# Optimization experiments

Measured on AMD Instinct MI355X. Metric: run time of the kernel, lower is better.

The kernel has to match this reference:

```python
import jax, jax.numpy as jnp
import numpy as np

B, CIN, COUT, N = 8, 64, 64, 4096
MODES, L, M = 64, 100, 20


def _cc_nodes_weights(m):
    # Clenshaw-Curtis nodes cos(k*pi/n) and weights on [-1, 1]
    n = m - 1
    k = np.arange(m)
    nodes = np.cos(np.pi * k / n)
    v = np.ones(m)
    for j in range(1, n // 2 + 1):
        b = 1.0 if 2 * j == n else 2.0
        v -= b / (4.0 * j * j - 1.0) * np.cos(2.0 * j * k * np.pi / n)
    w = 2.0 * v / n
    w[0] *= 0.5
    w[-1] *= 0.5
    return nodes, w


def setup_inputs() -> dict:
    key = jax.random.key(0)
    k1, k2, k3 = jax.random.split(key, 3)
    scale = 1.0 / (CIN * COUT)
    x = jax.random.normal(k1, (B, CIN, N), dtype=jnp.float32)
    w_real = scale * jax.random.uniform(k2, (CIN, COUT, MODES), dtype=jnp.float32)
    w_imag = scale * jax.random.uniform(k3, (CIN, COUT, MODES), dtype=jnp.float32)
    return {"x": x, "w_real": w_real, "w_imag": w_imag}


def _forward(x, w_real, w_imag):
    b, c, n = x.shape
    t = jnp.linspace(0.0, 1.0, n)
    f = np.fft.fftfreq(n, d=1.0 / n).astype(np.float32)  # integer freqs, fft order
    nodes, cw = _cc_nodes_weights(M)

    # ---- CFT: X(f) = sum_{segments l, cheb nodes k} w_lk * x(t_lk) * exp(-2i*pi*f*t_lk)
    h = 0.5 / L                               # segment half-width on [0,1]
    cents = (np.arange(L) + 0.5) / L
    t_nodes = (cents[:, None] + h * nodes[None, :]).ravel().astype(np.float32)  # (L*M,)
    wts = np.broadcast_to(h * cw, (L, M)).ravel().astype(np.float32)            # (L*M,)
    tq = jnp.asarray(t_nodes)
    # interpolate each (b, c) signal onto the Chebyshev quadrature nodes
    xs = jax.vmap(lambda s: jnp.interp(tq, t, s))(x.reshape(b * c, n))  # (BC, LM)
    phase = -2.0 * jnp.pi * jnp.asarray(f)[:, None] * tq[None, :]       # (N, LM)
    E = jnp.exp(1j * phase).astype(jnp.complex64) * jnp.asarray(wts)[None, :]
    x_cft = (xs.astype(jnp.complex64) @ E.T).reshape(b, c, n)           # (B, Cin, N)

    # ---- spectral channel mixing on lowest MODES fft-order frequencies
    w = (w_real + 1j * w_imag).astype(jnp.complex64)
    out_low = jnp.einsum('bix,iox->box', x_cft[:, :, :MODES], w)
    out_ft = jnp.concatenate(
        [out_low, jnp.zeros((b, COUT, n - MODES), dtype=jnp.complex64)], axis=-1)

    # ---- ICFT: x(t) = int X(f) exp(+2i*pi*f*t) df via the same segment quadrature
    order = np.argsort(f)
    f_sorted = f[order]
    cs = out_ft[:, :, jnp.asarray(order)].reshape(b * COUT, n)
    fa, fb = float(f_sorted[0]), float(f_sorted[-1])
    hf = (fb - fa) / (2.0 * L)
    fc = fa + (np.arange(L) + 0.5) * (fb - fa) / L
    f_nodes = (fc[:, None] + hf * nodes[None, :]).ravel().astype(np.float32)
    wfs = np.broadcast_to(hf * cw, (L, M)).ravel().astype(np.float32)
    fq = jnp.asarray(f_nodes)
    fs = jnp.asarray(f_sorted)
    ci = jax.vmap(lambda cv: jnp.interp(fq, fs, cv.real)
                  + 1j * jnp.interp(fq, fs, cv.imag))(cs)               # (BC, LM)
    phase2 = 2.0 * jnp.pi * fq[:, None] * t[None, :]                     # (LM, N)
    E2 = jnp.exp(1j * phase2).astype(jnp.complex64) * jnp.asarray(wfs)[:, None]
    return (ci.astype(jnp.complex64) @ E2).real.reshape(b, COUT, n)


def reference(x, w_real, w_imag):
    return _forward(x, w_real, w_imag)
```

## Files before the change

kernel.cpp:

```cpp
#include <hip/hip_runtime.h>


#define NN 4096
#define C1_19 0.9863613034027223
#define NS3 33
#define NSP 40
#define MAGIC 0x7fc0deadu

#define OFF_XRE 0
#define OFF_XIM 32768
#define OFF_Z   65536

__device__ __forceinline__ float sin_rev(float r) { return __builtin_amdgcn_sinf(r); }
__device__ __forceinline__ float cos_rev(float r) { return __builtin_amdgcn_cosf(r); }

__device__ __forceinline__ void build_tables(double* nd, double* cwd, int t) {
    if (t == 0) {
        nd[0] = 1.0; nd[1] = C1_19;
        for (int k = 2; k < 20; ++k) nd[k] = 2.0 * C1_19 * nd[k - 1] - nd[k - 2];
    }
    __syncthreads();
    if (t < 20) {
        double v = 1.0;
        for (int j = 1; j <= 9; ++j) {
            int q = (2 * j * t) % 38; if (q > 19) q = 38 - q;
            v -= 2.0 / (4.0 * j * j - 1.0) * nd[q];
        }
        double w = 2.0 * v / 19.0;
        if (t == 0 || t == 19) w *= 0.5;
        cwd[t] = w;
    }
}

struct PA { float xs[NN]; float xq[2000]; float Fri[20][64][2]; float red[4][64][2]; };
struct PB { float wsl[2][64][64]; float part[4][2][64]; float yt[2][64]; };
union SU { PA a; PB b; };

__global__ __launch_bounds__(256, 4) void k_cftmix(const float* __restrict__ x,
                                                   const float* __restrict__ wr,
                                                   const float* __restrict__ wi,
                                                   float* __restrict__ ws,
                                                   float* __restrict__ out) {
    __shared__ SU su;
    __shared__ double nd[20], cwd[20];
    __shared__ float sw0[NS3], sw1[NS3];
    __shared__ int   si0[NS3], si1[NS3];
    const int t = threadIdx.x;
    const int vb = blockIdx.x;

    if (vb < 512) {
        const int bc = vb;
        build_tables(nd, cwd, t);
#pragma unroll
        for (int it = 0; it < 4; ++it) {
            int c4 = it * 256 + t;
            *(float4*)&su.a.xs[c4 * 4] = *(const float4*)&x[(size_t)bc * NN + c4 * 4];
        }
        __syncthreads();
        for (int idx = t; idx < 1280; idx += 256) {
            int k = idx >> 6, m = idx & 63;
            double r = -0.005 * nd[k] * (double)m;
            r -= floor(r);
            float fr = (float)r;
            float w = (float)(0.005 * cwd[k]);
            su.a.Fri[k][m][0] = w * cos_rev(fr);
            su.a.Fri[k][m][1] = w * sin_rev(fr);
        }
#pragma unroll
        for (int it = 0; it < 8; ++it) {
            int node = it * 256 + t;
            if (node < 2000) {
                int l = node / 20, k = node - l * 20;
                double tq = 0.005 * ((double)(2 * l + 1) + nd[k]);
                double sf = tq * 4095.0;
                int i = (int)sf; if (i > 4094) i = 4094;
                double a = sf - (double)i;
                if (a < 0.0) a = 0.0; if (a > 1.0) a = 1.0;
                float af = (float)a;
                su.a.xq[node] = (1.f - af) * su.a.xs[i] + af * su.a.xs[i + 1];
            }
        }
        __syncthreads();
        const int m = t & 63, grp = t >> 6;
        float Fre[20], Fim[20];
#pragma unroll
        for (int k = 0; k < 20; ++k) {
            Fre[k] = su.a.Fri[k][m][0];
            Fim[k] = su.a.Fri[k][m][1];
        }
        float ar = 0.f, ai = 0.f;
        for (int l = grp * 25; l < grp * 25 + 25; ++l) {
            const float4* q4 = (const float4*)&su.a.xq[l * 20];
            float ur = 0.f, ui = 0.f;
#pragma unroll
            for (int c = 0; c < 5; ++c) {
                float4 q = q4[c];
                ur += q.x * Fre[c * 4]     + q.y * Fre[c * 4 + 1]
                    + q.z * Fre[c * 4 + 2] + q.w * Fre[c * 4 + 3];
                ui += q.x * Fim[c * 4]     + q.y * Fim[c * 4 + 1]
                    + q.z * Fim[c * 4 + 2] + q.w * Fim[c * 4 + 3];
            }
            int u = (m * (2 * l + 1)) % 200;
            float fr = (float)u * 0.005f;
            float tr = cos_rev(fr), ti = -sin_rev(fr);
            ar += tr * ur - ti * ui;
            ai += tr * ui + ti * ur;
        }
        su.a.red[grp][m][0] = ar;
        su.a.red[grp][m][1] = ai;
        __syncthreads();
        if (t < 64) {
            float sr = (su.a.red[0][t][0] + su.a.red[1][t][0]) +
                       (su.a.red[2][t][0] + su.a.red[3][t][0]);
            float si = (su.a.red[0][t][1] + su.a.red[1][t][1]) +
                       (su.a.red[2][t][1] + su.a.red[3][t][1]);
            __hip_atomic_store(&ws[OFF_XRE + (size_t)bc * 64 + t], sr,
                               __ATOMIC_RELAXED, __HIP_MEMORY_SCOPE_SYSTEM);
            __hip_atomic_store(&ws[OFF_XIM + (size_t)bc * 64 + t], si,
                               __ATOMIC_RELAXED, __HIP_MEMORY_SCOPE_SYSTEM);
        }
        __syncthreads();
        if (t == 0)
            __hip_atomic_store((unsigned*)out + (size_t)bc * 16, MAGIC,
                               __ATOMIC_RELAXED, __HIP_MEMORY_SCOPE_SYSTEM);
    } else {
        const int id = vb - 512;
        const int b = id >> 6, o = id & 63;
        build_tables(nd, cwd, t);
        __syncthreads();
        if (t < NS3) {
            int l = (t < 2) ? 49 : (t < 22 ? 50 : 51);
            int k = (t < 2) ? t : (t < 22 ? t - 2 : t - 13);
            double fq = -2048.0 + ((double)l + 0.5) * 40.95 + 20.475 * nd[k];
            int m0 = (int)floor(fq);
            float fr = (float)(fq - (double)m0);
            sw0[t] = (m0 >= 0 && m0 <= 63) ? (1.f - fr) : 0.f;
            sw1[t] = (m0 + 1 >= 0 && m0 + 1 <= 63) ? fr : 0.f;
            si0[t] = min(max(m0, 0), 63);
            si1[t] = min(max(m0 + 1, 0), 63);
        }
        for (int idx = t; idx < 2048; idx += 256) {
            int arr = idx >> 10, rem = idx & 1023;
            int i = rem >> 4, c4 = rem & 15;
            const float* src = arr ? wi : wr;
            *(float4*)&su.b.wsl[arr][i][c4 * 4] =
                *(const float4*)&src[(((size_t)i * 64 + o) << 6) + c4 * 4];
        }
        if (t < 64) {
            const unsigned* fp = (const unsigned*)out + (size_t)(b * 64 + t) * 16;
            while (__hip_atomic_load(fp, __ATOMIC_RELAXED,
                                     __HIP_MEMORY_SCOPE_SYSTEM) != MAGIC)
                __builtin_amdgcn_s_sleep(2);
        }
        __syncthreads();
        const int m = t & 63, grp = t >> 6;
        float yr = 0.f, yi = 0.f;
#pragma unroll 4
        for (int i = grp * 16; i < grp * 16 + 16; ++i) {
            const size_t off = (size_t)(b * 64 + i) * 64 + m;
            float xr = ws[OFF_XRE + off];
            float xi = ws[OFF_XIM + off];
            float a = su.b.wsl[0][i][m];
            float c = su.b.wsl[1][i][m];
            yr += xr * a - xi * c;
            yi += xr * c + xi * a;
        }
        su.b.part[grp][0][m] = yr;
        su.b.part[grp][1][m] = yi;
        __syncthreads();
        if (t < 128) {
            int pr = t >> 6, mm = t & 63;
            su.b.yt[pr][mm] = ((su.b.part[0][pr][mm] + su.b.part[1][pr][mm]) +
                               (su.b.part[2][pr][mm] + su.b.part[3][pr][mm]));
        }
        __syncthreads();
        if (t < 2 * NS3) {
            int p = t >= NS3, s = t - p * NS3;
            float z = sw0[s] * su.b.yt[p][si0[s]] + sw1[s] * su.b.yt[p][si1[s]];
            ws[OFF_Z + (size_t)p * 512 * NSP + ((size_t)b * 64 + o) * NSP + s] = z;
        } else if (t < 2 * NS3 + 14) {
            int q = t - 2 * NS3;
            int p = q / 7, s = NS3 + q % 7;
            ws[OFF_Z + (size_t)p * 512 * NSP + ((size_t)b * 64 + o) * NSP + s] = 0.f;
        }
    }
}

__global__ __launch_bounds__(256) void k_icft(const float* __restrict__ ws,
                                              float* __restrict__ out) {
    __shared__ double nd[20], cwd[20];
    __shared__ double sfq[NS3];
    __shared__ float  swf[NS3];
    __shared__ __align__(16) float zt[2][64][41];
    __shared__ __align__(16) float e2[2][NSP][36];
    const int t = threadIdx.x;
    const int jt2 = blockIdx.x, pc = blockIdx.y;
    build_tables(nd, cwd, t);
    __syncthreads();
    if (t < NS3) {
        int l = (t < 2) ? 49 : (t < 22 ? 50 : 51);
        int k = (t < 2) ? t : (t < 22 ? t - 2 : t - 13);
        sfq[t] = -2048.0 + ((double)l + 0.5) * 40.95 + 20.475 * nd[k];
        swf[t] = (float)(20.475 * cwd[k]);
    }
    for (int idx = t; idx < 2 * 64 * NSP; idx += 256) {
        int part = idx / (64 * NSP), rem = idx % (64 * NSP);
        int row = rem / NSP, s = rem % NSP;
        zt[part][row][s] =
            ws[OFF_Z + (size_t)part * 512 * NSP + ((size_t)pc * 64 + row) * NSP + s];
    }
    __syncthreads();
    const double inv4095 = 1.0 / 4095.0;
    for (int idx = t; idx < NSP * 32; idx += 256) {
        int s = idx >> 5, jl = idx & 31;
        float cr = 0.f, ci = 0.f;
        if (s < NS3) {
            double ph = sfq[s] * ((double)(jt2 * 32 + jl) * inv4095);
            ph -= floor(ph);
            float fr = (float)ph;
            cr = swf[s] * cos_rev(fr);
            ci = swf[s] * sin_rev(fr);
        }
        e2[0][s][jl] = cr;
        e2[1][s][jl] = ci;
    }
    __syncthreads();
    const int jg = t & 7, pg = t >> 3;
    float acc[2][4] = {{0.f}};
    for (int s0 = 0; s0 < NSP; s0 += 8) {
        float zr[2][8], zi[2][8];
#pragma unroll
        for (int p = 0; p < 2; ++p)
#pragma unroll
            for (int v = 0; v < 8; ++v) {
                zr[p][v] = zt[0][pg * 2 + p][s0 + v];
                zi[p][v] = zt[1][pg * 2 + p][s0 + v];
            }
#pragma unroll
        for (int v = 0; v < 8; ++v) {
            const float4 er = *(const float4*)&e2[0][s0 + v][jg * 4];
            const float4 ei = *(const float4*)&e2[1][s0 + v][jg * 4];
#pragma unroll
            for (int p = 0; p < 2; ++p) {
                acc[p][0] += zr[p][v] * er.x - zi[p][v] * ei.x;
                acc[p][1] += zr[p][v] * er.y - zi[p][v] * ei.y;
                acc[p][2] += zr[p][v] * er.z - zi[p][v] * ei.z;
                acc[p][3] += zr[p][v] * er.w - zi[p][v] * ei.w;
            }
        }
    }
#pragma unroll
    for (int p = 0; p < 2; ++p) {
        float4 r;
        r.x = acc[p][0]; r.y = acc[p][1]; r.z = acc[p][2]; r.w = acc[p][3];
        *(float4*)&out[(size_t)(pc * 64 + pg * 2 + p) * NN + jt2 * 32 + jg * 4] = r;
    }
}

extern "C" void kernel_launch(void* const* d_in, const int* in_sizes, int n_in,
                              void* d_out, int out_size, void* d_ws, size_t ws_size,
                              hipStream_t stream) {
    const float* x  = (const float*)d_in[0];
    const float* wr = (const float*)d_in[1];
    const float* wi = (const float*)d_in[2];
    float* out = (float*)d_out;
    float* ws  = (float*)d_ws;
    (void)in_sizes; (void)n_in; (void)out_size; (void)ws_size;

    k_cftmix<<<1024, 256, 0, stream>>>(x, wr, wi, ws, out);
    k_icft<<<dim3(128, 8), 256, 0, stream>>>(ws, out);
}
```

Measured before the change: 29.91 us.

## Merge CFT and mixing roles into one block; widen ICFT row tile

The CFT producer blocks and the spectral-mixing consumer blocks become a single set of 512 blocks. Each block computes its own (b,c) CFT, publishes it through a flag, then spin-waits on the 64 flags of its batch before mixing for output channel o. The weight slice is prefetched into registers during the CFT phase, and the per-segment twiddle index becomes an incremental update instead of a modulo. The ICFT kernel now handles 128 rows per block with four rows per thread, halving the grid to improve reuse of the exponential table. The in-kernel grid barrier assumes all 512 blocks are co-resident, and register pressure rises because the launch-bounds occupancy hint was removed and wbuf adds 32 live registers.

```diff
diff --git a/kernel.cpp b/kernel.cpp
--- a/kernel.cpp
+++ b/kernel.cpp
@@ -32,157 +32,163 @@
     }
 }
 
-struct PA { float xs[NN]; float xq[2000]; float Fri[20][64][2]; float red[4][64][2]; };
-struct PB { float wsl[2][64][64]; float part[4][2][64]; float yt[2][64]; };
-union SU { PA a; PB b; };
-
-__global__ __launch_bounds__(256, 4) void k_cftmix(const float* __restrict__ x,
-                                                   const float* __restrict__ wr,
-                                                   const float* __restrict__ wi,
-                                                   float* __restrict__ ws,
-                                                   float* __restrict__ out) {
-    __shared__ SU su;
+union EU {
+    struct { float xs[NN]; float xq[2000]; float Fri[20][64][2]; } a;
+    float wsl[2][64][64];
+};
+
+__global__ __launch_bounds__(256) void k_cftmix(const float* __restrict__ x,
+                                                const float* __restrict__ wr,
+                                                const float* __restrict__ wi,
+                                                float* __restrict__ ws,
+                                                float* __restrict__ out) {
+    __shared__ EU eu;
     __shared__ double nd[20], cwd[20];
+    __shared__ float red[4][64][2];
+    __shared__ float part[4][2][64];
+    __shared__ float yt[2][64];
     __shared__ float sw0[NS3], sw1[NS3];
     __shared__ int   si0[NS3], si1[NS3];
     const int t = threadIdx.x;
-    const int vb = blockIdx.x;
-
-    if (vb < 512) {
-        const int bc = vb;
-        build_tables(nd, cwd, t);
-#pragma unroll
-        for (int it = 0; it < 4; ++it) {
-            int c4 = it * 256 + t;
-            *(float4*)&su.a.xs[c4 * 4] = *(const float4*)&x[(size_t)bc * NN + c4 * 4];
-        }
-        __syncthreads();
-        for (int idx = t; idx < 1280; idx += 256) {
-            int k = idx >> 6, m = idx & 63;
-            double r = -0.005 * nd[k] * (double)m;
-            r -= floor(r);
-            float fr = (float)r;
-            float w = (float)(0.005 * cwd[k]);
-            su.a.Fri[k][m][0] = w * cos_rev(fr);
-            su.a.Fri[k][m][1] = w * sin_rev(fr);
-        }
-#pragma unroll
-        for (int it = 0; it < 8; ++it) {
-            int node = it * 256 + t;
-            if (node < 2000) {
-                int l = node / 20, k = node - l * 20;
-                double tq = 0.005 * ((double)(2 * l + 1) + nd[k]);
-                double sf = tq * 4095.0;
-                int i = (int)sf; if (i > 4094) i = 4094;
-                double a = sf - (double)i;
-                if (a < 0.0) a = 0.0; if (a > 1.0) a = 1.0;
-                float af = (float)a;
-                su.a.xq[node] = (1.f - af) * su.a.xs[i] + af * su.a.xs[i + 1];
-            }
-        }
-        __syncthreads();
-        const int m = t & 63, grp = t >> 6;
-        float Fre[20], Fim[20];
-#pragma unroll
-        for (int k = 0; k < 20; ++k) {
-            Fre[k] = su.a.Fri[k][m][0];
-            Fim[k] = su.a.Fri[k][m][1];
-        }
-        float ar = 0.f, ai = 0.f;
-        for (int l = grp * 25; l < grp * 25 + 25; ++l) {
-            const float4* q4 = (const float4*)&su.a.xq[l * 20];
-            float ur = 0.f, ui = 0.f;
-#pragma unroll
-            for (int c = 0; c < 5; ++c) {
-                float4 q = q4[c];
-                ur += q.x * Fre[c * 4]     + q.y * Fre[c * 4 + 1]
-                    + q.z * Fre[c * 4 + 2] + q.w * Fre[c * 4 + 3];
-                ui += q.x * Fim[c * 4]     + q.y * Fim[c * 4 + 1]
-                    + q.z * Fim[c * 4 + 2] + q.w * Fim[c * 4 + 3];
-            }
-            int u = (m * (2 * l + 1)) % 200;
-            float fr = (float)u * 0.005f;
-            float tr = cos_rev(fr), ti = -sin_rev(fr);
-            ar += tr * ur - ti * ui;
-            ai += tr * ui + ti * ur;
-        }
-        su.a.red[grp][m][0] = ar;
-        su.a.red[grp][m][1] = ai;
-        __syncthreads();
-        if (t < 64) {
-            float sr = (su.a.red[0][t][0] + su.a.red[1][t][0]) +
-                       (su.a.red[2][t][0] + su.a.red[3][t][0]);
-            float si = (su.a.red[0][t][1] + su.a.red[1][t][1]) +
-                       (su.a.red[2][t][1] + su.a.red[3][t][1]);
-            __hip_atomic_store(&ws[OFF_XRE + (size_t)bc * 64 + t], sr,
-                               __ATOMIC_RELAXED, __HIP_MEMORY_SCOPE_SYSTEM);
-            __hip_atomic_store(&ws[OFF_XIM + (size_t)bc * 64 + t], si,
-                               __ATOMIC_RELAXED, __HIP_MEMORY_SCOPE_SYSTEM);
-        }
-        __syncthreads();
-        if (t == 0)
-            __hip_atomic_store((unsigned*)out + (size_t)bc * 16, MAGIC,
-                               __ATOMIC_RELAXED, __HIP_MEMORY_SCOPE_SYSTEM);
-    } else {
-        const int id = vb - 512;
-        const int b = id >> 6, o = id & 63;
-        build_tables(nd, cwd, t);
-        __syncthreads();
-        if (t < NS3) {
-            int l = (t < 2) ? 49 : (t < 22 ? 50 : 51);
-            int k = (t < 2) ? t : (t < 22 ? t - 2 : t - 13);
-            double fq = -2048.0 + ((double)l + 0.5) * 40.95 + 20.475 * nd[k];
-            int m0 = (int)floor(fq);
-            float fr = (float)(fq - (double)m0);
-            sw0[t] = (m0 >= 0 && m0 <= 63) ? (1.f - fr) : 0.f;
-            sw1[t] = (m0 + 1 >= 0 && m0 + 1 <= 63) ? fr : 0.f;
-            si0[t] = min(max(m0, 0), 63);
-            si1[t] = min(max(m0 + 1, 0), 63);
-        }
-        for (int idx = t; idx < 2048; idx += 256) {
-            int arr = idx >> 10, rem = idx & 1023;
-            int i = rem >> 4, c4 = rem & 15;
-            const float* src = arr ? wi : wr;
-            *(float4*)&su.b.wsl[arr][i][c4 * 4] =
-                *(const float4*)&src[(((size_t)i * 64 + o) << 6) + c4 * 4];
-        }
-        if (t < 64) {
-            const unsigned* fp = (const unsigned*)out + (size_t)(b * 64 + t) * 16;
-            while (__hip_atomic_load(fp, __ATOMIC_RELAXED,
-                                     __HIP_MEMORY_SCOPE_SYSTEM) != MAGIC)
-                __builtin_amdgcn_s_sleep(2);
-        }
-        __syncthreads();
-        const int m = t & 63, grp = t >> 6;
+    const int bc = blockIdx.x;
+    const int b = bc >> 6, o = bc & 63;
+
+    build_tables(nd, cwd, t);
+#pragma unroll
+    for (int it = 0; it < 4; ++it) {
+        int c4 = it * 256 + t;
+        *(float4*)&eu.a.xs[c4 * 4] = *(const float4*)&x[(size_t)bc * NN + c4 * 4];
+    }
+    __syncthreads();
+    if (t < NS3) {
+        int l = (t < 2) ? 49 : (t < 22 ? 50 : 51);
+        int k = (t < 2) ? t : (t < 22 ? t - 2 : t - 13);
+        double fq = -2048.0 + ((double)l + 0.5) * 40.95 + 20.475 * nd[k];
+        int m0 = (int)floor(fq);
+        float fr = (float)(fq - (double)m0);
+        sw0[t] = (m0 >= 0 && m0 <= 63) ? (1.f - fr) : 0.f;
+        sw1[t] = (m0 + 1 >= 0 && m0 + 1 <= 63) ? fr : 0.f;
+        si0[t] = min(max(m0, 0), 63);
+        si1[t] = min(max(m0 + 1, 0), 63);
+    }
+    for (int idx = t; idx < 1280; idx += 256) {
+        int k = idx >> 6, m = idx & 63;
+        double r = -0.005 * nd[k] * (double)m;
+        r -= floor(r);
+        float fr = (float)r;
+        float w = (float)(0.005 * cwd[k]);
+        eu.a.Fri[k][m][0] = w * cos_rev(fr);
+        eu.a.Fri[k][m][1] = w * sin_rev(fr);
+    }
+#pragma unroll
+    for (int it = 0; it < 8; ++it) {
+        int node = it * 256 + t;
+        if (node < 2000) {
+            int l = node / 20, k = node - l * 20;
+            double tq = 0.005 * ((double)(2 * l + 1) + nd[k]);
+            double sf = tq * 4095.0;
+            int i = (int)sf; if (i > 4094) i = 4094;
+            double a = sf - (double)i;
+            if (a < 0.0) a = 0.0; if (a > 1.0) a = 1.0;
+            float af = (float)a;
+            eu.a.xq[node] = (1.f - af) * eu.a.xs[i] + af * eu.a.xs[i + 1];
+        }
+    }
+    __syncthreads();
+    float4 wbuf[8];
+#pragma unroll
+    for (int c = 0; c < 8; ++c) {
+        int f = c * 256 + t;
+        int arr = f >> 10, rem = f & 1023;
+        int i = rem >> 4, m4 = rem & 15;
+        const float* src = arr ? wi : wr;
+        wbuf[c] = *(const float4*)&src[(((size_t)i * 64 + o) << 6) + m4 * 4];
+    }
+    const int m = t & 63, grp = t >> 6;
+    float Fre[20], Fim[20];
+#pragma unroll
+    for (int k = 0; k < 20; ++k) {
+        Fre[k] = eu.a.Fri[k][m][0];
+        Fim[k] = eu.a.Fri[k][m][1];
+    }
+    float ar = 0.f, ai = 0.f;
+    int u = (m * (50 * grp + 1)) % 200;
+    const int du = 2 * m;
+    for (int l = grp * 25; l < grp * 25 + 25; ++l) {
+        const float4* q4 = (const float4*)&eu.a.xq[l * 20];
+        float ur = 0.f, ui = 0.f;
+#pragma unroll
+        for (int c = 0; c < 5; ++c) {
+            float4 q = q4[c];
+            ur += q.x * Fre[c * 4]     + q.y * Fre[c * 4 + 1]
+                + q.z * Fre[c * 4 + 2] + q.w * Fre[c * 4 + 3];
+            ui += q.x * Fim[c * 4]     + q.y * Fim[c * 4 + 1]
+                + q.z * Fim[c * 4 + 2] + q.w * Fim[c * 4 + 3];
+        }
+        float fr = (float)u * 0.005f;
+        float tr = cos_rev(fr), ti = -sin_rev(fr);
+        ar += tr * ur - ti * ui;
+        ai += tr * ui + ti * ur;
+        u += du; if (u >= 200) u -= 200;
+    }
+    red[grp][m][0] = ar;
+    red[grp][m][1] = ai;
+    __syncthreads();
+    {
+        float4* wf = (float4*)&eu.wsl[0][0][0];
+#pragma unroll
+        for (int c = 0; c < 8; ++c)
+            wf[c * 256 + t] = wbuf[c];
+    }
+    if (t < 64) {
+        float sr = (red[0][t][0] + red[1][t][0]) + (red[2][t][0] + red[3][t][0]);
+        float si = (red[0][t][1] + red[1][t][1]) + (red[2][t][1] + red[3][t][1]);
+        __hip_atomic_store(&ws[OFF_XRE + (size_t)bc * 64 + t], sr,
+                           __ATOMIC_RELAXED, __HIP_MEMORY_SCOPE_SYSTEM);
+        __hip_atomic_store(&ws[OFF_XIM + (size_t)bc * 64 + t], si,
+                           __ATOMIC_RELAXED, __HIP_MEMORY_SCOPE_SYSTEM);
+    }
+    __syncthreads();
+    if (t == 0)
+        __hip_atomic_store((unsigned*)out + (size_t)bc * 16, MAGIC,
+                           __ATOMIC_RELAXED, __HIP_MEMORY_SCOPE_SYSTEM);
+    if (t < 64) {
+        const unsigned* fp = (const unsigned*)out + (size_t)(b * 64 + t) * 16;
+        while (__hip_atomic_load(fp, __ATOMIC_RELAXED,
+                                 __HIP_MEMORY_SCOPE_SYSTEM) != MAGIC)
+            __builtin_amdgcn_s_sleep(2);
+    }
+    __syncthreads();
+    {
         float yr = 0.f, yi = 0.f;
 #pragma unroll 4
         for (int i = grp * 16; i < grp * 16 + 16; ++i) {
             const size_t off = (size_t)(b * 64 + i) * 64 + m;
             float xr = ws[OFF_XRE + off];
             float xi = ws[OFF_XIM + off];
-            float a = su.b.wsl[0][i][m];
-            float c = su.b.wsl[1][i][m];
+            float a = eu.wsl[0][i][m];
+            float c = eu.wsl[1][i][m];
             yr += xr * a - xi * c;
             yi += xr * c + xi * a;
         }
-        su.b.part[grp][0][m] = yr;
-        su.b.part[grp][1][m] = yi;
-        __syncthreads();
-        if (t < 128) {
-            int pr = t >> 6, mm = t & 63;
-            su.b.yt[pr][mm] = ((su.b.part[0][pr][mm] + su.b.part[1][pr][mm]) +
-                               (su.b.part[2][pr][mm] + su.b.part[3][pr][mm]));
-        }
-        __syncthreads();
-        if (t < 2 * NS3) {
-            int p = t >= NS3, s = t - p * NS3;
-            float z = sw0[s] * su.b.yt[p][si0[s]] + sw1[s] * su.b.yt[p][si1[s]];
-            ws[OFF_Z + (size_t)p * 512 * NSP + ((size_t)b * 64 + o) * NSP + s] = z;
-        } else if (t < 2 * NS3 + 14) {
-            int q = t - 2 * NS3;
-            int p = q / 7, s = NS3 + q % 7;
-            ws[OFF_Z + (size_t)p * 512 * NSP + ((size_t)b * 64 + o) * NSP + s] = 0.f;
-        }
+        part[grp][0][m] = yr;
+        part[grp][1][m] = yi;
+    }
+    __syncthreads();
+    if (t < 128) {
+        int pr = t >> 6, mm = t & 63;
+        yt[pr][mm] = ((part[0][pr][mm] + part[1][pr][mm]) +
+                      (part[2][pr][mm] + part[3][pr][mm]));
+    }
+    __syncthreads();
+    if (t < 2 * NS3) {
+        int p = t >= NS3, s = t - p * NS3;
+        float z = sw0[s] * yt[p][si0[s]] + sw1[s] * yt[p][si1[s]];
+        ws[OFF_Z + (size_t)p * 512 * NSP + ((size_t)b * 64 + o) * NSP + s] = z;
+    } else if (t < 2 * NS3 + 14) {
+        int q = t - 2 * NS3;
+        int p = q / 7, s = NS3 + q % 7;
+        ws[OFF_Z + (size_t)p * 512 * NSP + ((size_t)b * 64 + o) * NSP + s] = 0.f;
     }
 }
 
@@ -191,10 +197,10 @@
     __shared__ double nd[20], cwd[20];
     __shared__ double sfq[NS3];
     __shared__ float  swf[NS3];
-    __shared__ __align__(16) float zt[2][64][41];
+    __shared__ float  zt[2][128][41];
     __shared__ __align__(16) float e2[2][NSP][36];
     const int t = threadIdx.x;
-    const int jt2 = blockIdx.x, pc = blockIdx.y;
+    const int jt2 = blockIdx.x, pcc = blockIdx.y;
     build_tables(nd, cwd, t);
     __syncthreads();
     if (t < NS3) {
@@ -203,11 +209,11 @@
         sfq[t] = -2048.0 + ((double)l + 0.5) * 40.95 + 20.475 * nd[k];
         swf[t] = (float)(20.475 * cwd[k]);
     }
-    for (int idx = t; idx < 2 * 64 * NSP; idx += 256) {
-        int part = idx / (64 * NSP), rem = idx % (64 * NSP);
+    for (int idx = t; idx < 2 * 128 * NSP; idx += 256) {
+        int part = idx / (128 * NSP), rem = idx % (128 * NSP);
         int row = rem / NSP, s = rem % NSP;
         zt[part][row][s] =
-            ws[OFF_Z + (size_t)part * 512 * NSP + ((size_t)pc * 64 + row) * NSP + s];
+            ws[OFF_Z + (size_t)part * 512 * NSP + ((size_t)pcc * 128 + row) * NSP + s];
     }
     __syncthreads();
     const double inv4095 = 1.0 / 4095.0;
@@ -226,22 +232,22 @@
     }
     __syncthreads();
     const int jg = t & 7, pg = t >> 3;
-    float acc[2][4] = {{0.f}};
+    float acc[4][4] = {{0.f}};
     for (int s0 = 0; s0 < NSP; s0 += 8) {
-        float zr[2][8], zi[2][8];
-#pragma unroll
-        for (int p = 0; p < 2; ++p)
+        float zr[4][8], zi[4][8];
+#pragma unroll
+        for (int p = 0; p < 4; ++p)
 #pragma unroll
             for (int v = 0; v < 8; ++v) {
-                zr[p][v] = zt[0][pg * 2 + p][s0 + v];
-                zi[p][v] = zt[1][pg * 2 + p][s0 + v];
+                zr[p][v] = zt[0][pg * 4 + p][s0 + v];
+                zi[p][v] = zt[1][pg * 4 + p][s0 + v];
             }
 #pragma unroll
         for (int v = 0; v < 8; ++v) {
             const float4 er = *(const float4*)&e2[0][s0 + v][jg * 4];
             const float4 ei = *(const float4*)&e2[1][s0 + v][jg * 4];
 #pragma unroll
-            for (int p = 0; p < 2; ++p) {
+            for (int p = 0; p < 4; ++p) {
                 acc[p][0] += zr[p][v] * er.x - zi[p][v] * ei.x;
                 acc[p][1] += zr[p][v] * er.y - zi[p][v] * ei.y;
                 acc[p][2] += zr[p][v] * er.z - zi[p][v] * ei.z;
@@ -250,10 +256,10 @@
         }
     }
 #pragma unroll
-    for (int p = 0; p < 2; ++p) {
+    for (int p = 0; p < 4; ++p) {
         float4 r;
         r.x = acc[p][0]; r.y = acc[p][1]; r.z = acc[p][2]; r.w = acc[p][3];
-        *(float4*)&out[(size_t)(pc * 64 + pg * 2 + p) * NN + jt2 * 32 + jg * 4] = r;
+        *(float4*)&out[(size_t)(pcc * 128 + pg * 4 + p) * NN + jt2 * 32 + jg * 4] = r;
     }
 }
 
@@ -267,6 +273,6 @@
     float* ws  = (float*)d_ws;
     (void)in_sizes; (void)n_in; (void)out_size; (void)ws_size;
 
-    k_cftmix<<<1024, 256, 0, stream>>>(x, wr, wi, ws, out);
-    k_icft<<<dim3(128, 8), 256, 0, stream>>>(ws, out);
-}
+    k_cftmix<<<512, 256, 0, stream>>>(x, wr, wi, ws, out);
+    k_icft<<<dim3(128, 4), 256, 0, stream>>>(ws, out);
+}
```

Measured after the change: 35.45 us. +18.5%, slower.
